# Kernel tuning notes

Measured on AMD Instinct MI355X. Metric: run time of the kernel, lower is better.

Reference implementation:

```python
import jax, jax.numpy as jnp
from jax import lax
import numpy as np

KERNEL_SIZE = 29
N_T = 1000
SIGMA_MIN, SIGMA_MAX = 0.5, 20.0
HIDDEN = 32


def _gaussian_kernel1d(sigma, ksize):
    # torchvision: linspace over [-half, half], normalized gaussian pdf
    half = (ksize - 1) * 0.5
    xg = jnp.linspace(-half, half, ksize)
    pdf = jnp.exp(-0.5 * (xg / sigma) ** 2)
    return pdf / pdf.sum()


def batch_blur(x, sigmas, ksize=KERNEL_SIZE):
    # x: [B,C,H,W], sigmas: [B]. Per-sample separable gaussian blur as a single
    # grouped depthwise conv (feature_group_count = B*C) instead of a Python loop.
    B, C, H, W = x.shape
    k1 = jax.vmap(lambda s: _gaussian_kernel1d(s, ksize))(sigmas)  # [B, k]
    pad = ksize // 2
    xp = jnp.pad(x, ((0, 0), (0, 0), (pad, pad), (pad, pad)), mode='reflect')
    lhs = xp.reshape(1, B * C, H + 2 * pad, W + 2 * pad)
    kbc = jnp.repeat(k1, C, axis=0)  # [B*C, k] per-channel kernel
    # vertical pass then horizontal pass (outer-product 2D kernel == two 1D passes)
    y = lax.conv_general_dilated(lhs, kbc[:, None, :, None], (1, 1), 'VALID',
                                 feature_group_count=B * C)
    y = lax.conv_general_dilated(y, kbc[:, None, None, :], (1, 1), 'VALID',
                                 feature_group_count=B * C)
    return y.reshape(B, C, H, W)


def gt_net(z, tn, W1, b1, tw, W2, b2):
    # simple time-conditioned conv net standing in for the opaque `gt` module
    h = lax.conv_general_dilated(z, W1, (1, 1), 'SAME')  # [B,HIDDEN,H,W]
    h = h + b1[None, :, None, None] + (tn[:, None] * tw[None, :])[:, :, None, None]
    h = jax.nn.relu(h)
    out = lax.conv_general_dilated(h, W2, (1, 1), 'SAME') + b2[None, :, None, None]
    return out


def setup_inputs() -> dict:
    key = jax.random.key(0)
    ks = jax.random.split(key, 6)
    B, C, H, W = 32, 3, 256, 256
    x = jax.random.normal(ks[0], (B, C, H, W), dtype=jnp.float32)
    t = jax.random.randint(ks[1], (B,), 0, N_T, dtype=jnp.int32)
    W1 = jax.random.normal(ks[2], (HIDDEN, C, 3, 3), dtype=jnp.float32) * 0.1
    b1 = jnp.zeros((HIDDEN,), dtype=jnp.float32)
    tw = jax.random.normal(ks[3], (HIDDEN,), dtype=jnp.float32) * 0.1
    W2 = jax.random.normal(ks[4], (C, HIDDEN, 3, 3), dtype=jnp.float32) * 0.1
    b2 = jnp.zeros((C,), dtype=jnp.float32)
    sigma_schedule = jnp.linspace(SIGMA_MIN, SIGMA_MAX, N_T, dtype=jnp.float32)
    return {"x": x, "t": t, "W1": W1, "b1": b1, "tw": tw, "W2": W2, "b2": b2,
            "sigma_schedule": sigma_schedule}


def reference(x, t, W1, b1, tw, W2, b2, sigma_schedule):
    sigma_t = sigma_schedule[t]                      # [B]
    z_t = batch_blur(x, sigma_t, KERNEL_SIZE)        # [B,C,H,W]
    preds = gt_net(z_t, t.astype(jnp.float32) / N_T, W1, b1, tw, W2, b2)
    return jnp.mean((x - preds) ** 2)                # MSELoss
```

## Files before the change

kernel.cpp:

```cpp
#include <hip/hip_runtime.h>
#include <hip/hip_bf16.h>

#define BATCH 32
#define CH 3
#define HH 256
#define WW 256
#define KS 29
#define PAD 14
#define NT_F 1000.0f

typedef __attribute__((ext_vector_type(8))) short short8;
typedef __attribute__((ext_vector_type(4))) float f32x4;

union U4 { short8 s8; uint4 u4; };

__device__ inline unsigned short bf16rne(float f) {
  unsigned u = __float_as_uint(f);
  unsigned r = (u + 0x7FFFu + ((u >> 16) & 1u)) >> 16;
  return (unsigned short)r;
}
__device__ inline unsigned pk_bf16(float a, float b) {
  union { __hip_bfloat162 h2; unsigned u; } cv;
  cv.h2 = __float22bfloat162_rn(make_float2(a, b));
  return cv.u;
}


#define PARTIAL_OFF 3150656

__global__ void prep_kernel(const float* __restrict__ sched,
                            const int* __restrict__ t,
                            const float* __restrict__ W1,
                            const float* __restrict__ b1,
                            const float* __restrict__ tw,
                            const float* __restrict__ W2,
                            float* __restrict__ ws) {
  int tid = threadIdx.x;
  float* gk = ws;
  float* tcond = ws + 1024;
  unsigned short* w1k = (unsigned short*)(ws + 2048);
  unsigned short* w1g = (unsigned short*)(ws + 2560);
  unsigned short* w2c = (unsigned short*)(ws + 2624);
  if (tid < BATCH) {
    float sigma = sched[t[tid]];
    float inv = 1.0f / sigma;
    float wv[KS];
    float s = 0.0f;
#pragma unroll
    for (int i = 0; i < KS; i++) {
      float xg = (float)(i - PAD) * inv;
      wv[i] = expf(-0.5f * xg * xg);
      s += wv[i];
    }
    float rs = 1.0f / s;
#pragma unroll
    for (int i = 0; i < KS; i++) gk[tid * 32 + i] = wv[i] * rs;
  }
  for (int i = tid; i < 1024; i += 256) {
    int o = i >> 5, k = i & 31;
    int q = k >> 3, j = k & 7, ci = j & 3;
    int dy, dx;
    if (q < 3) { dy = q; dx = j >> 2; } else { dy = j >> 2; dx = 2; }
    w1k[i] = (ci < 3) ? bf16rne(W1[o * 27 + ci * 9 + dy * 3 + dx]) : (unsigned short)0;
  }
  for (int i = tid; i < 128; i += 256) {
    int o = i >> 2, j = i & 3;
    w1g[i] = (j < 3) ? bf16rne(W1[o * 27 + j * 9 + 8]) : (unsigned short)0;
  }
  for (int i = tid; i < 4608; i += 256) {
    int tap = i >> 9, r = i & 511;
    int n = r >> 5, kn = r & 31;
    int och = (kn >> 1) + ((kn & 1) ? 16 : 0);
    int dy = tap / 3, dx = tap - dy * 3;
    w2c[i] = (n < 3) ? bf16rne(W2[((n * 32 + och) * 3 + dy) * 3 + dx])
                     : (unsigned short)0;
  }
  for (int i = tid; i < 1024; i += 256) {
    int b = i >> 5, o = i & 31;
    tcond[i] = b1[o] + ((float)t[b] * (1.0f / NT_F)) * tw[o];
  }
}

__global__ __launch_bounds__(256, 3) void blur_kernel(const float* __restrict__ x,
                                                      const float* __restrict__ ws,
                                                      unsigned short* __restrict__ z) {
  __shared__ float vsp[32][288];
  int blk = blockIdx.x;
  int rg = blk & 7;
  int bc = blk >> 3;
  int b = bc / CH;
  int y0 = rg * 32;
  int tid = threadIdx.x;
  const float* xp = x + (size_t)bc * (HH * WW);
  const float* kb = ws + b * 32;

  float xv[60];
#pragma unroll
  for (int i = 0; i < 60; i++) {
    int gy = y0 - PAD + i;
    gy = (gy < 0) ? -gy : gy;
    gy = (gy >= HH) ? (2 * HH - 2 - gy) : gy;
    xv[i] = xp[gy * WW + tid];
  }
  float acc[32];
#pragma unroll
  for (int yy = 0; yy < 32; yy++) acc[yy] = 0.0f;
#pragma unroll
  for (int kk = 0; kk < KS; kk++) {
    float kv = kb[kk];
#pragma unroll
    for (int yy = 0; yy < 32; yy++) acc[yy] += kv * xv[yy + kk];
  }
#pragma unroll
  for (int yy = 0; yy < 32; yy++) vsp[yy][tid + 16] = acc[yy];
  __syncthreads();
  {
    int row = tid >> 4, i2 = tid & 15;
#pragma unroll
    for (int r2 = 0; r2 < 2; r2++) {
      int rr = row + 16 * r2;
      vsp[rr][i2] = vsp[rr][32 - i2];
      vsp[rr][272 + i2] = vsp[rr][270 - i2];
    }
  }
  __syncthreads();

  size_t zb = (size_t)bc * (HH * WW);
#pragma unroll
  for (int it = 0; it < 8; ++it) {
    int unit = tid + 256 * it;
    int row = unit >> 6, cg = unit & 63;
    float w[36];
#pragma unroll
    for (int i = 0; i < 9; i++)
      *(float4*)&w[4 * i] = *(const float4*)&vsp[row][4 * (cg + i)];
    float o0 = 0, o1 = 0, o2 = 0, o3 = 0;
#pragma unroll
    for (int kk = 0; kk < KS; kk++) {
      float kv = kb[kk];
      o0 += kv * w[2 + kk];
      o1 += kv * w[3 + kk];
      o2 += kv * w[4 + kk];
      o3 += kv * w[5 + kk];
    }
    unsigned u0 = pk_bf16(o0, o1);
    unsigned u1 = pk_bf16(o2, o3);
    *(uint2*)&z[zb + (size_t)(y0 + row) * WW + 4 * cg] = make_uint2(u0, u1);
  }
}

__global__ __launch_bounds__(256, 5) void convloss_kernel(
    const float* __restrict__ x, const float* __restrict__ ws,
    const float* __restrict__ b2g, float* __restrict__ partial) {
  __shared__ __align__(16) unsigned short zs4[400 * 4];
  __shared__ __align__(16) unsigned short hs[324 * 40];
  __shared__ float wsum[4];

  const float* tcond = ws + 1024;
  const unsigned short* w1k = (const unsigned short*)(ws + 2048);
  const unsigned short* w1g = (const unsigned short*)(ws + 2560);
  const unsigned short* w2c = (const unsigned short*)(ws + 2624);
  const unsigned short* zg = (const unsigned short*)(ws + 4928);

  int bx = blockIdx.x, by = blockIdx.y, b = blockIdx.z;
  int tid = threadIdx.x;
  int x0 = bx * 16, y0 = by * 16;
  const unsigned short* zbp = zg + (size_t)b * 3 * HH * WW;

  int lane = tid & 63;
  int q = lane >> 4;
  int col = lane & 15;
  int wv = tid >> 6;

#pragma unroll
  for (int r = 0; r < 2; r++) {
    int unit = tid + 256 * r;
    if (unit < 400) {
      int zy = unit / 20, zx = unit - zy * 20;
      int gy = y0 - 2 + zy, gx = x0 - 2 + zx;
      unsigned c0 = 0, c1 = 0, c2 = 0;
      if ((unsigned)gy < (unsigned)HH && (unsigned)gx < (unsigned)WW) {
        int gi = gy * WW + gx;
        c0 = zbp[gi];
        c1 = zbp[HH * WW + gi];
        c2 = zbp[2 * HH * WW + gi];
      }
      *(uint2*)&zs4[unit * 4] = make_uint2(c0 | (c1 << 16), c2);
    }
  }

  const float* xb = x + (size_t)b * 3 * HH * WW;
  int colc = (col < 3) ? col : 0;
  float4 xpre[4];
#pragma unroll
  for (int i = 0; i < 4; i++) {
    int g2 = wv * 4 + i;
    xpre[i] = *(const float4*)&xb[colc * (HH * WW) + (y0 + g2) * WW + x0 + q * 4];
  }

  U4 B1a, B1b, B2a, B2b;
  B1a.u4 = *(const uint4*)(w1k + col * 32 + q * 8);
  B1b.u4 = *(const uint4*)(w1k + (col + 16) * 32 + q * 8);
  {
    uint2 ta = *(const uint2*)(w1g + col * 4);
    uint2 tb = *(const uint2*)(w1g + (col + 16) * 4);
    bool q0 = (q == 0);
    B2a.u4 = make_uint4(q0 ? ta.x : 0u, q0 ? ta.y : 0u, 0u, 0u);
    B2b.u4 = make_uint4(q0 ? tb.x : 0u, q0 ? tb.y : 0u, 0u, 0u);
  }
  float tc0 = tcond[b * 32 + col];
  float tc1 = tcond[b * 32 + 16 + col];
  float b2v = b2g[colc];

  __syncthreads();

  const f32x4 zero4 = {0.0f, 0.0f, 0.0f, 0.0f};
  int dyq = (q < 3) ? q : 0;
  int dxq = (q < 3) ? 0 : 2;
  int strB = (q < 3) ? 4 : 80;

#pragma unroll
  for (int i = 0; i < 6; i++) {
    int g = wv + 4 * i;
    if (g < 21) {
      int p = g * 16 + col;
      if (p > 323) p = 323;
      int py = p / 18, px = p - py * 18;
      int a0 = ((py + dyq) * 20 + px + dxq) * 4;
      uint2 lo = *(const uint2*)&zs4[a0];
      uint2 hi = *(const uint2*)&zs4[a0 + strB];
      U4 A1;
      A1.u4 = make_uint4(lo.x, lo.y, hi.x, hi.y);
      uint2 t2 = *(const uint2*)&zs4[((py + 2) * 20 + px + 2) * 4];
      U4 A2;
      bool q0 = (q == 0);
      A2.u4 = make_uint4(q0 ? t2.x : 0u, q0 ? t2.y : 0u, 0u, 0u);
      f32x4 acc0 = __builtin_amdgcn_mfma_f32_16x16x32_bf16(A1.s8, B1a.s8, zero4, 0, 0, 0);
      acc0 = __builtin_amdgcn_mfma_f32_16x16x32_bf16(A2.s8, B2a.s8, acc0, 0, 0, 0);
      f32x4 acc1 = __builtin_amdgcn_mfma_f32_16x16x32_bf16(A1.s8, B1b.s8, zero4, 0, 0, 0);
      acc1 = __builtin_amdgcn_mfma_f32_16x16x32_bf16(A2.s8, B2b.s8, acc1, 0, 0, 0);
      int prow = g * 16 + q * 4;
#pragma unroll
      for (int r = 0; r < 4; r++) {
        int pw = prow + r;
        if (pw < 324) {
          unsigned pk = pk_bf16(fmaxf(acc0[r] + tc0, 0.0f),
                                fmaxf(acc1[r] + tc1, 0.0f));
          *(unsigned*)&hs[pw * 40 + 2 * col] = pk;
        }
      }
    }
  }
  __syncthreads();

  f32x4 dacc[4];
#pragma unroll
  for (int i = 0; i < 4; i++) dacc[i] = zero4;
#pragma unroll
  for (int tap = 0; tap < 9; tap++) {
    const int dy = tap / 3, dx = tap - (tap / 3) * 3;
    U4 Bt;
    Bt.u4 = *(const uint4*)(w2c + tap * 512 + col * 32 + q * 8);
#pragma unroll
    for (int i = 0; i < 4; i++) {
      int g2 = wv * 4 + i;
      int p18 = (g2 + dy) * 18 + (col + dx);
      U4 A;
      A.u4 = *(const uint4*)&hs[p18 * 40 + q * 8];
      dacc[i] = __builtin_amdgcn_mfma_f32_16x16x32_bf16(A.s8, Bt.s8, dacc[i], 0, 0, 0);
    }
  }

  float s = 0.0f;
  if (col < 3) {
#pragma unroll
    for (int i = 0; i < 4; i++) {
      float4 xv = xpre[i];
      float d0 = xv.x - (dacc[i][0] + b2v);
      float d1 = xv.y - (dacc[i][1] + b2v);
      float d2 = xv.z - (dacc[i][2] + b2v);
      float d3 = xv.w - (dacc[i][3] + b2v);
      s += d0 * d0 + d1 * d1 + d2 * d2 + d3 * d3;
    }
  }
#pragma unroll
  for (int off = 32; off > 0; off >>= 1) s += __shfl_down(s, off);
  if (lane == 0) wsum[wv] = s;
  __syncthreads();
  if (tid == 0) {
    int bid = (b * 16 + by) * 16 + bx;
    partial[bid] = wsum[0] + wsum[1] + wsum[2] + wsum[3];
  }
}

__global__ __launch_bounds__(256) void reduce_kernel(const float* __restrict__ partial,
                                                     float* __restrict__ out) {
  __shared__ float wsum[4];
  int tid = threadIdx.x;
  float s = 0.0f;
#pragma unroll
  for (int i = 0; i < 8; i++) {
    float4 v = *(const float4*)&partial[(tid + 256 * i) * 4];
    s += v.x + v.y + v.z + v.w;
  }
#pragma unroll
  for (int off = 32; off > 0; off >>= 1) s += __shfl_down(s, off);
  if ((tid & 63) == 0) wsum[tid >> 6] = s;
  __syncthreads();
  if (tid == 0)
    out[0] = (wsum[0] + wsum[1] + wsum[2] + wsum[3]) * (1.0f / 6291456.0f);
}

extern "C" void kernel_launch(void* const* d_in, const int* in_sizes, int n_in,
                              void* d_out, int out_size, void* d_ws, size_t ws_size,
                              hipStream_t stream) {
  const float* x = (const float*)d_in[0];
  const int* t = (const int*)d_in[1];
  const float* W1 = (const float*)d_in[2];
  const float* b1 = (const float*)d_in[3];
  const float* tw = (const float*)d_in[4];
  const float* W2 = (const float*)d_in[5];
  const float* b2 = (const float*)d_in[6];
  const float* sched = (const float*)d_in[7];
  float* out = (float*)d_out;
  float* ws = (float*)d_ws;
  unsigned short* z = (unsigned short*)(ws + 4928);
  float* partial = ws + PARTIAL_OFF;

  prep_kernel<<<1, 256, 0, stream>>>(sched, t, W1, b1, tw, W2, ws);
  blur_kernel<<<BATCH * CH * 8, 256, 0, stream>>>(x, ws, z);
  dim3 grid(16, 16, BATCH);
  convloss_kernel<<<grid, 256, 0, stream>>>(x, ws, b2, partial);
  reduce_kernel<<<1, 256, 0, stream>>>(partial, out);
}
```

Measured before the change: 146.8 us.

## Fold prep into blur kernel and simplify convloss hidden-tile indexing

The separate prep launch is removed. Each blur block now computes its own Gaussian taps in shared memory via a wave reduction, and one extra block builds the bf16 weight tables and time-conditioning terms. In convloss, the hidden tile is laid out with a 20-wide row pitch so pixel addressing needs no divide or clamp. The bias and time-conditioning terms are now folded into the MFMA accumulator initial values. This cuts one launch and some ALU work, at the cost of more LDS per block, a lower occupancy hint (5 to 4), and 25 instead of 21 MFMA groups in the first conv stage.

```diff
diff --git a/kernel.cpp b/kernel.cpp
--- a/kernel.cpp
+++ b/kernel.cpp
@@ -28,71 +28,53 @@
 
 #define PARTIAL_OFF 3150656
 
-__global__ void prep_kernel(const float* __restrict__ sched,
-                            const int* __restrict__ t,
-                            const float* __restrict__ W1,
-                            const float* __restrict__ b1,
-                            const float* __restrict__ tw,
-                            const float* __restrict__ W2,
-                            float* __restrict__ ws) {
+__global__ __launch_bounds__(256, 3) void blur_kernel(
+    const float* __restrict__ x, const int* __restrict__ t,
+    const float* __restrict__ sched, const float* __restrict__ W1,
+    const float* __restrict__ b1, const float* __restrict__ tw,
+    const float* __restrict__ W2, float* __restrict__ ws,
+    unsigned short* __restrict__ z) {
+  int blk = blockIdx.x;
   int tid = threadIdx.x;
-  float* gk = ws;
-  float* tcond = ws + 1024;
-  unsigned short* w1k = (unsigned short*)(ws + 2048);
-  unsigned short* w1g = (unsigned short*)(ws + 2560);
-  unsigned short* w2c = (unsigned short*)(ws + 2624);
-  if (tid < BATCH) {
-    float sigma = sched[t[tid]];
-    float inv = 1.0f / sigma;
-    float wv[KS];
-    float s = 0.0f;
-#pragma unroll
-    for (int i = 0; i < KS; i++) {
-      float xg = (float)(i - PAD) * inv;
-      wv[i] = expf(-0.5f * xg * xg);
-      s += wv[i];
-    }
-    float rs = 1.0f / s;
-#pragma unroll
-    for (int i = 0; i < KS; i++) gk[tid * 32 + i] = wv[i] * rs;
-  }
-  for (int i = tid; i < 1024; i += 256) {
-    int o = i >> 5, k = i & 31;
-    int q = k >> 3, j = k & 7, ci = j & 3;
-    int dy, dx;
-    if (q < 3) { dy = q; dx = j >> 2; } else { dy = j >> 2; dx = 2; }
-    w1k[i] = (ci < 3) ? bf16rne(W1[o * 27 + ci * 9 + dy * 3 + dx]) : (unsigned short)0;
-  }
-  for (int i = tid; i < 128; i += 256) {
-    int o = i >> 2, j = i & 3;
-    w1g[i] = (j < 3) ? bf16rne(W1[o * 27 + j * 9 + 8]) : (unsigned short)0;
-  }
-  for (int i = tid; i < 4608; i += 256) {
-    int tap = i >> 9, r = i & 511;
-    int n = r >> 5, kn = r & 31;
-    int och = (kn >> 1) + ((kn & 1) ? 16 : 0);
-    int dy = tap / 3, dx = tap - dy * 3;
-    w2c[i] = (n < 3) ? bf16rne(W2[((n * 32 + och) * 3 + dy) * 3 + dx])
-                     : (unsigned short)0;
-  }
-  for (int i = tid; i < 1024; i += 256) {
-    int b = i >> 5, o = i & 31;
-    tcond[i] = b1[o] + ((float)t[b] * (1.0f / NT_F)) * tw[o];
-  }
-}
-
-__global__ __launch_bounds__(256, 3) void blur_kernel(const float* __restrict__ x,
-                                                      const float* __restrict__ ws,
-                                                      unsigned short* __restrict__ z) {
+
+  if (blk >= BATCH * CH * 8) {
+    float* tcond = ws + 1024;
+    unsigned short* w1k = (unsigned short*)(ws + 2048);
+    unsigned short* w1g = (unsigned short*)(ws + 2560);
+    unsigned short* w2c = (unsigned short*)(ws + 2624);
+    for (int i = tid; i < 1024; i += 256) {
+      int o = i >> 5, k = i & 31;
+      int q = k >> 3, j = k & 7, ci = j & 3;
+      int dy, dx;
+      if (q < 3) { dy = q; dx = j >> 2; } else { dy = j >> 2; dx = 2; }
+      w1k[i] = (ci < 3) ? bf16rne(W1[o * 27 + ci * 9 + dy * 3 + dx]) : (unsigned short)0;
+    }
+    for (int i = tid; i < 128; i += 256) {
+      int o = i >> 2, j = i & 3;
+      w1g[i] = (j < 3) ? bf16rne(W1[o * 27 + j * 9 + 8]) : (unsigned short)0;
+    }
+    for (int i = tid; i < 4608; i += 256) {
+      int tap = i >> 9, r = i & 511;
+      int n = r >> 5, kn = r & 31;
+      int och = (kn >> 1) + ((kn & 1) ? 16 : 0);
+      int dy = tap / 3, dx = tap - dy * 3;
+      w2c[i] = (n < 3) ? bf16rne(W2[((n * 32 + och) * 3 + dy) * 3 + dx])
+                       : (unsigned short)0;
+    }
+    for (int i = tid; i < 1024; i += 256) {
+      int b = i >> 5, o = i & 31;
+      tcond[i] = b1[o] + ((float)t[b] * (1.0f / NT_F)) * tw[o];
+    }
+    return;
+  }
+
   __shared__ float vsp[32][288];
-  int blk = blockIdx.x;
+  __shared__ float gkl[32];
   int rg = blk & 7;
   int bc = blk >> 3;
   int b = bc / CH;
   int y0 = rg * 32;
-  int tid = threadIdx.x;
   const float* xp = x + (size_t)bc * (HH * WW);
-  const float* kb = ws + b * 32;
 
   float xv[60];
 #pragma unroll
@@ -102,12 +84,28 @@
     gy = (gy >= HH) ? (2 * HH - 2 - gy) : gy;
     xv[i] = xp[gy * WW + tid];
   }
+
+  if (tid < 64) {
+    float wexp = 0.0f;
+    if (tid < KS) {
+      float sigma = sched[t[b]];
+      float xg = (float)(tid - PAD) / sigma;
+      wexp = expf(-0.5f * xg * xg);
+    }
+    float s = wexp;
+#pragma unroll
+    for (int off = 32; off > 0; off >>= 1) s += __shfl_down(s, off);
+    float tot = __shfl(s, 0);
+    if (tid < 32) gkl[tid] = wexp / tot;
+  }
+  __syncthreads();
+
   float acc[32];
 #pragma unroll
   for (int yy = 0; yy < 32; yy++) acc[yy] = 0.0f;
 #pragma unroll
   for (int kk = 0; kk < KS; kk++) {
-    float kv = kb[kk];
+    float kv = gkl[kk];
 #pragma unroll
     for (int yy = 0; yy < 32; yy++) acc[yy] += kv * xv[yy + kk];
   }
@@ -137,7 +135,7 @@
     float o0 = 0, o1 = 0, o2 = 0, o3 = 0;
 #pragma unroll
     for (int kk = 0; kk < KS; kk++) {
-      float kv = kb[kk];
+      float kv = gkl[kk];
       o0 += kv * w[2 + kk];
       o1 += kv * w[3 + kk];
       o2 += kv * w[4 + kk];
@@ -149,11 +147,11 @@
   }
 }
 
-__global__ __launch_bounds__(256, 5) void convloss_kernel(
+__global__ __launch_bounds__(256, 4) void convloss_kernel(
     const float* __restrict__ x, const float* __restrict__ ws,
     const float* __restrict__ b2g, float* __restrict__ partial) {
-  __shared__ __align__(16) unsigned short zs4[400 * 4];
-  __shared__ __align__(16) unsigned short hs[324 * 40];
+  __shared__ __align__(16) unsigned short zs4[448 * 4];
+  __shared__ __align__(16) unsigned short hs[400 * 40];
   __shared__ float wsum[4];
 
   const float* tcond = ws + 1024;
@@ -175,7 +173,7 @@
 #pragma unroll
   for (int r = 0; r < 2; r++) {
     int unit = tid + 256 * r;
-    if (unit < 400) {
+    if (unit < 448) {
       int zy = unit / 20, zx = unit - zy * 20;
       int gy = y0 - 2 + zy, gx = x0 - 2 + zx;
       unsigned c0 = 0, c1 = 0, c2 = 0;
@@ -211,51 +209,47 @@
   float tc0 = tcond[b * 32 + col];
   float tc1 = tcond[b * 32 + 16 + col];
   float b2v = b2g[colc];
-
-  __syncthreads();
-
-  const f32x4 zero4 = {0.0f, 0.0f, 0.0f, 0.0f};
+  const f32x4 tcv0 = {tc0, tc0, tc0, tc0};
+  const f32x4 tcv1 = {tc1, tc1, tc1, tc1};
+
+  __syncthreads();
+
   int dyq = (q < 3) ? q : 0;
   int dxq = (q < 3) ? 0 : 2;
-  int strB = (q < 3) ? 4 : 80;
-
-#pragma unroll
-  for (int i = 0; i < 6; i++) {
+  int strBpx = (q < 3) ? 1 : 20;
+  int baseoff = dyq * 20 + dxq;
+
+#pragma unroll
+  for (int i = 0; i < 7; i++) {
     int g = wv + 4 * i;
-    if (g < 21) {
+    if (g < 25) {
       int p = g * 16 + col;
-      if (p > 323) p = 323;
-      int py = p / 18, px = p - py * 18;
-      int a0 = ((py + dyq) * 20 + px + dxq) * 4;
-      uint2 lo = *(const uint2*)&zs4[a0];
-      uint2 hi = *(const uint2*)&zs4[a0 + strB];
+      uint2 lo = *(const uint2*)&zs4[(p + baseoff) * 4];
+      uint2 hi = *(const uint2*)&zs4[(p + baseoff + strBpx) * 4];
       U4 A1;
       A1.u4 = make_uint4(lo.x, lo.y, hi.x, hi.y);
-      uint2 t2 = *(const uint2*)&zs4[((py + 2) * 20 + px + 2) * 4];
+      uint2 t2 = *(const uint2*)&zs4[(p + 42) * 4];
       U4 A2;
       bool q0 = (q == 0);
       A2.u4 = make_uint4(q0 ? t2.x : 0u, q0 ? t2.y : 0u, 0u, 0u);
-      f32x4 acc0 = __builtin_amdgcn_mfma_f32_16x16x32_bf16(A1.s8, B1a.s8, zero4, 0, 0, 0);
+      f32x4 acc0 = __builtin_amdgcn_mfma_f32_16x16x32_bf16(A1.s8, B1a.s8, tcv0, 0, 0, 0);
       acc0 = __builtin_amdgcn_mfma_f32_16x16x32_bf16(A2.s8, B2a.s8, acc0, 0, 0, 0);
-      f32x4 acc1 = __builtin_amdgcn_mfma_f32_16x16x32_bf16(A1.s8, B1b.s8, zero4, 0, 0, 0);
+      f32x4 acc1 = __builtin_amdgcn_mfma_f32_16x16x32_bf16(A1.s8, B1b.s8, tcv1, 0, 0, 0);
       acc1 = __builtin_amdgcn_mfma_f32_16x16x32_bf16(A2.s8, B2b.s8, acc1, 0, 0, 0);
       int prow = g * 16 + q * 4;
 #pragma unroll
       for (int r = 0; r < 4; r++) {
-        int pw = prow + r;
-        if (pw < 324) {
-          unsigned pk = pk_bf16(fmaxf(acc0[r] + tc0, 0.0f),
-                                fmaxf(acc1[r] + tc1, 0.0f));
-          *(unsigned*)&hs[pw * 40 + 2 * col] = pk;
-        }
+        unsigned pk = pk_bf16(fmaxf(acc0[r], 0.0f), fmaxf(acc1[r], 0.0f));
+        *(unsigned*)&hs[(prow + r) * 40 + 2 * col] = pk;
       }
     }
   }
   __syncthreads();
 
+  const f32x4 bcv = {b2v, b2v, b2v, b2v};
   f32x4 dacc[4];
 #pragma unroll
-  for (int i = 0; i < 4; i++) dacc[i] = zero4;
+  for (int i = 0; i < 4; i++) dacc[i] = bcv;
 #pragma unroll
   for (int tap = 0; tap < 9; tap++) {
     const int dy = tap / 3, dx = tap - (tap / 3) * 3;
@@ -263,10 +257,9 @@
     Bt.u4 = *(const uint4*)(w2c + tap * 512 + col * 32 + q * 8);
 #pragma unroll
     for (int i = 0; i < 4; i++) {
-      int g2 = wv * 4 + i;
-      int p18 = (g2 + dy) * 18 + (col + dx);
+      int p20 = (wv * 4 + i + dy) * 20 + (col + dx);
       U4 A;
-      A.u4 = *(const uint4*)&hs[p18 * 40 + q * 8];
+      A.u4 = *(const uint4*)&hs[p20 * 40 + q * 8];
       dacc[i] = __builtin_amdgcn_mfma_f32_16x16x32_bf16(A.s8, Bt.s8, dacc[i], 0, 0, 0);
     }
   }
@@ -276,10 +269,10 @@
 #pragma unroll
     for (int i = 0; i < 4; i++) {
       float4 xv = xpre[i];
-      float d0 = xv.x - (dacc[i][0] + b2v);
-      float d1 = xv.y - (dacc[i][1] + b2v);
-      float d2 = xv.z - (dacc[i][2] + b2v);
-      float d3 = xv.w - (dacc[i][3] + b2v);
+      float d0 = xv.x - dacc[i][0];
+      float d1 = xv.y - dacc[i][1];
+      float d2 = xv.z - dacc[i][2];
+      float d3 = xv.w - dacc[i][3];
       s += d0 * d0 + d1 * d1 + d2 * d2 + d3 * d3;
     }
   }
@@ -327,8 +320,7 @@
   unsigned short* z = (unsigned short*)(ws + 4928);
   float* partial = ws + PARTIAL_OFF;
 
-  prep_kernel<<<1, 256, 0, stream>>>(sched, t, W1, b1, tw, W2, ws);
-  blur_kernel<<<BATCH * CH * 8, 256, 0, stream>>>(x, ws, z);
+  blur_kernel<<<BATCH * CH * 8 + 1, 256, 0, stream>>>(x, t, sched, W1, b1, tw, W2, ws, z);
   dim3 grid(16, 16, BATCH);
   convloss_kernel<<<grid, 256, 0, stream>>>(x, ws, b2, partial);
   reduce_kernel<<<1, 256, 0, stream>>>(partial, out);
```

Result: no change. 145.8 us (-0.7%).
